# Performance work log

Measured on AMD Instinct MI355X. Metric: run time of the kernel, lower is better.

## Reference

```python
import jax, jax.numpy as jnp
import numpy as np

IN_F = 2048
OUT_F = 2048
BATCH = 16384
BASE_SPARSITY = 0.02
REVIVAL_DENSITY = 0.2   # rows for dead ('low') output neurons
RELIEF_DENSITY = 0.15   # cols for saturated ('high') input neurons
DEAD = np.arange(16)                      # 'low' extrema (row indices)
SATURATED = np.arange(100, 900, 100)      # 'high' extrema (col indices)


def _make_mask(key):
    k1, k2, k3 = jax.random.split(key, 3)
    base = (jax.random.uniform(k1, (OUT_F, IN_F)) < BASE_SPARSITY).astype(jnp.float32)
    patch = jnp.zeros((OUT_F, IN_F), jnp.float32)
    # dense-ish rows for dead output neurons
    row_patch = (jax.random.uniform(k2, (len(DEAD), IN_F)) < REVIVAL_DENSITY).astype(jnp.float32)
    patch = patch.at[jnp.asarray(DEAD), :].set(row_patch)
    # dense-ish cols for saturated input neurons (overwrite, matching torch order)
    col_patch = (jax.random.uniform(k3, (OUT_F, len(SATURATED))) < RELIEF_DENSITY).astype(jnp.float32)
    patch = patch.at[:, jnp.asarray(SATURATED)].set(col_patch)
    return jnp.maximum(base, patch)


def setup_inputs() -> dict:
    key = jax.random.key(0)
    kx, kw, km = jax.random.split(key, 3)
    x = jax.random.normal(kx, (BATCH, IN_F), dtype=jnp.float32)
    # kaiming_uniform_(a=sqrt(5)) -> U(-bound, bound), bound = sqrt(6/((1+a^2)*fan_in)) = 1/sqrt(fan_in)
    bound = 1.0 / np.sqrt(IN_F)
    weight = jax.random.uniform(kw, (OUT_F, IN_F), minval=-bound, maxval=bound, dtype=jnp.float32)
    bias = jnp.zeros((OUT_F,), jnp.float32)
    mask = _make_mask(km)
    return {"x": x, "weight": weight, "bias": bias, "mask": mask}


def reference(x, weight, bias, mask):
    # F.linear(x, weight * mask, bias): y = x @ (W*M)^T + b
    return jnp.einsum('bi,oi->bo', x, weight * mask) + bias
```

## Files before the change

kernel.cpp:

```cpp
#include <hip/hip_runtime.h>
#include <stdint.h>

#define BATCH 16384
#define IN_F 2048
#define OUT_F 2048

typedef unsigned short u16;
typedef __attribute__((ext_vector_type(8))) short bf16x8;
typedef __attribute__((ext_vector_type(4))) float f32x4;

__device__ __forceinline__ u16 f2bf(float f) {
  union { float f; uint32_t u; } v; v.f = f;
  uint32_t u = v.u;
  u += 0x7FFFu + ((u >> 16) & 1u);
  return (u16)(u >> 16);
}


__global__ void cvt_x_kernel(const float4* __restrict__ x, u16* __restrict__ out) {
  int i = blockIdx.x * 256 + threadIdx.x;
  float4 v = x[i];
  uint2 p;
  p.x = (uint32_t)f2bf(v.x) | ((uint32_t)f2bf(v.y) << 16);
  p.y = (uint32_t)f2bf(v.z) | ((uint32_t)f2bf(v.w) << 16);
  ((uint2*)out)[i] = p;
}

__global__ void cvt_w_kernel(const float4* __restrict__ w, const float4* __restrict__ m,
                             u16* __restrict__ out) {
  int i = blockIdx.x * 256 + threadIdx.x;
  float4 wv = w[i];
  float4 mv = m[i];
  uint2 p;
  p.x = (uint32_t)f2bf(wv.x * mv.x) | ((uint32_t)f2bf(wv.y * mv.y) << 16);
  p.y = (uint32_t)f2bf(wv.z * mv.z) | ((uint32_t)f2bf(wv.w * mv.w) << 16);
  ((uint2*)out)[i] = p;
}


__device__ __forceinline__ void async_cp16(const void* g, void* l) {
  __builtin_amdgcn_global_load_lds(
      (const __attribute__((address_space(1))) void*)g,
      (__attribute__((address_space(3))) void*)l,
      16, 0, 0);
}


__global__ __launch_bounds__(256) void gemm_bf16(const u16* __restrict__ A,
                                                 const u16* __restrict__ B,
                                                 const float* __restrict__ bias,
                                                 float* __restrict__ C) {
  __shared__ u16 lsA[128 * 32];
  __shared__ u16 lsB[128 * 32];
  const int K = IN_F, N = OUT_F;
  const int tid = threadIdx.x;
  const int lane = tid & 63, wave = tid >> 6;
  const int waveM = (wave & 1) * 64, waveN = (wave >> 1) * 64;
  const long bm = (long)blockIdx.x * 128;
  const long bn = (long)blockIdx.y * 128;

  const int o1 = tid * 16;
  const int o2 = o1 + 4096;
  const int r1 = tid >> 2, r2 = r1 + 64;
  const int c = tid & 3;
  const int cs1 = c ^ ((r1 >> 1) & 3);
  const int cs2 = c ^ ((r2 >> 1) & 3);
  const u16* gA1 = A + (bm + r1) * K + cs1 * 8;
  const u16* gA2 = A + (bm + r2) * K + cs2 * 8;
  const u16* gB1 = B + (bn + r1) * K + cs1 * 8;
  const u16* gB2 = B + (bn + r2) * K + cs2 * 8;
  char* lA1 = (char*)lsA + o1;
  char* lA2 = (char*)lsA + o2;
  char* lB1 = (char*)lsB + o1;
  char* lB2 = (char*)lsB + o2;

  f32x4 acc[4][4];
#pragma unroll
  for (int i = 0; i < 4; i++)
#pragma unroll
    for (int j = 0; j < 4; j++)
#pragma unroll
      for (int r = 0; r < 4; r++) acc[i][j][r] = 0.0f;

  const int mrow = lane & 15;
  const int q = lane >> 4;

  for (int k0 = 0; k0 < K; k0 += 32) {
    async_cp16(gA1 + k0, lA1);
    async_cp16(gA2 + k0, lA2);
    async_cp16(gB1 + k0, lB1);
    async_cp16(gB2 + k0, lB2);
    __syncthreads();

    bf16x8 af[4], bfr[4];
#pragma unroll
    for (int i = 0; i < 4; i++) {
      const int rr = waveM + i * 16 + mrow;
      af[i] = *(const bf16x8*)&lsA[rr * 32 + (q ^ ((rr >> 1) & 3)) * 8];
    }
#pragma unroll
    for (int j = 0; j < 4; j++) {
      const int rr = waveN + j * 16 + mrow;
      bfr[j] = *(const bf16x8*)&lsB[rr * 32 + (q ^ ((rr >> 1) & 3)) * 8];
    }

#pragma unroll
    for (int i = 0; i < 4; i++)
#pragma unroll
      for (int j = 0; j < 4; j++)
        acc[i][j] = __builtin_amdgcn_mfma_f32_16x16x32_bf16(af[i], bfr[j], acc[i][j], 0, 0, 0);

    __syncthreads();
  }

  const int cn = lane & 15;
  const int crow = (lane >> 4) * 4;
#pragma unroll
  for (int j = 0; j < 4; j++) {
    const long n = bn + waveN + j * 16 + cn;
    const float bv = bias[n];
#pragma unroll
    for (int i = 0; i < 4; i++) {
      const long m0 = bm + waveM + i * 16 + crow;
      float* cp = C + m0 * N + n;
#pragma unroll
      for (int r = 0; r < 4; r++)
        cp[(long)r * N] = acc[i][j][r] + bv;
    }
  }
}


__global__ void naive_kernel(const float* __restrict__ x, const float* __restrict__ w,
                             const float* __restrict__ bias, const float* __restrict__ m,
                             float* __restrict__ out) {
  size_t idx = (size_t)blockIdx.x * 256 + threadIdx.x;
  int o = (int)(idx % OUT_F);
  size_t b = idx / OUT_F;
  float s = bias[o];
  const float* xr = x + b * IN_F;
  const float* wr = w + (size_t)o * IN_F;
  const float* mr = m + (size_t)o * IN_F;
  for (int k = 0; k < IN_F; k++) s += xr[k] * wr[k] * mr[k];
  out[idx] = s;
}

extern "C" void kernel_launch(void* const* d_in, const int* in_sizes, int n_in,
                              void* d_out, int out_size, void* d_ws, size_t ws_size,
                              hipStream_t stream) {
  const float* x = (const float*)d_in[0];
  const float* w = (const float*)d_in[1];
  const float* bias = (const float*)d_in[2];
  const float* mask = (const float*)d_in[3];
  float* out = (float*)d_out;

  const size_t xb_elems = (size_t)BATCH * IN_F;
  const size_t wm_elems = (size_t)OUT_F * IN_F;
  const size_t need = (xb_elems + wm_elems) * sizeof(u16);

  if (ws_size >= need) {
    u16* xb = (u16*)d_ws;
    u16* wm = xb + xb_elems;
    cvt_x_kernel<<<(uint32_t)(xb_elems / 4 / 256), 256, 0, stream>>>((const float4*)x, xb);
    cvt_w_kernel<<<(uint32_t)(wm_elems / 4 / 256), 256, 0, stream>>>((const float4*)w,
                                                                     (const float4*)mask, wm);
    gemm_bf16<<<dim3(BATCH / 128, OUT_F / 128), 256, 0, stream>>>(xb, wm, bias, out);
  } else {
    naive_kernel<<<(uint32_t)(((size_t)BATCH * OUT_F) / 256), 256, 0, stream>>>(x, w, bias, mask, out);
  }
}
```

Before: 407.2 us.

## Fuse fp32-to-bf16 conversion of x into GEMM tile loading

Removes the separate pass that converted x to bf16 in workspace; the GEMM now async-copies fp32 x tiles into LDS and converts them to bf16 when building MFMA fragments. This avoids an extra full read and write of the large activation matrix, at the cost of doubled A-tile global/LDS traffic per block and extra pack instructions in the inner loop. Rounding changes from round-to-nearest-even to round-half-up.

```diff
diff --git a/kernel.cpp b/kernel.cpp
--- a/kernel.cpp
+++ b/kernel.cpp
@@ -16,15 +16,12 @@
   return (u16)(u >> 16);
 }
 
+__device__ __forceinline__ uint32_t pk_bf16(float a, float b) {
+  uint32_t ua = __float_as_uint(a) + 0x8000u;
+  uint32_t ub = __float_as_uint(b) + 0x8000u;
+  return __builtin_amdgcn_perm(ub, ua, 0x07060302u);
+}
 
-__global__ void cvt_x_kernel(const float4* __restrict__ x, u16* __restrict__ out) {
-  int i = blockIdx.x * 256 + threadIdx.x;
-  float4 v = x[i];
-  uint2 p;
-  p.x = (uint32_t)f2bf(v.x) | ((uint32_t)f2bf(v.y) << 16);
-  p.y = (uint32_t)f2bf(v.z) | ((uint32_t)f2bf(v.w) << 16);
-  ((uint2*)out)[i] = p;
-}
 
 __global__ void cvt_w_kernel(const float4* __restrict__ w, const float4* __restrict__ m,
                              u16* __restrict__ out) {
@@ -46,12 +43,12 @@
 }
 
 
-__global__ __launch_bounds__(256) void gemm_bf16(const u16* __restrict__ A,
+__global__ __launch_bounds__(256) void gemm_xf32(const float* __restrict__ A,
                                                  const u16* __restrict__ B,
                                                  const float* __restrict__ bias,
                                                  float* __restrict__ C) {
-  __shared__ u16 lsA[128 * 32];
-  __shared__ u16 lsB[128 * 32];
+  __shared__ float lsA[128 * 32];
+  __shared__ u16  lsB[128 * 32];
   const int K = IN_F, N = OUT_F;
   const int tid = threadIdx.x;
   const int lane = tid & 63, wave = tid >> 6;
@@ -59,20 +56,26 @@
   const long bm = (long)blockIdx.x * 128;
   const long bn = (long)blockIdx.y * 128;
 
-  const int o1 = tid * 16;
-  const int o2 = o1 + 4096;
-  const int r1 = tid >> 2, r2 = r1 + 64;
-  const int c = tid & 3;
-  const int cs1 = c ^ ((r1 >> 1) & 3);
-  const int cs2 = c ^ ((r2 >> 1) & 3);
-  const u16* gA1 = A + (bm + r1) * K + cs1 * 8;
-  const u16* gA2 = A + (bm + r2) * K + cs2 * 8;
-  const u16* gB1 = B + (bn + r1) * K + cs1 * 8;
-  const u16* gB2 = B + (bn + r2) * K + cs2 * 8;
-  char* lA1 = (char*)lsA + o1;
-  char* lA2 = (char*)lsA + o2;
-  char* lB1 = (char*)lsB + o1;
-  char* lB2 = (char*)lsB + o2;
+  const float* gA[4];
+  char* lA[4];
+#pragma unroll
+  for (int kk = 0; kk < 4; kk++) {
+    const int s = kk * 256 + tid;
+    const int r = s >> 3, c = s & 7;
+    const int cg = c ^ (r & 7);
+    gA[kk] = A + (bm + r) * K + cg * 4;
+    lA[kk] = (char*)lsA + s * 16;
+  }
+  const u16* gB[2];
+  char* lB[2];
+#pragma unroll
+  for (int kk = 0; kk < 2; kk++) {
+    const int s = kk * 256 + tid;
+    const int r = s >> 2, c = s & 3;
+    const int cg = c ^ ((r >> 1) & 3);
+    gB[kk] = B + (bn + r) * K + cg * 8;
+    lB[kk] = (char*)lsB + s * 16;
+  }
 
   f32x4 acc[4][4];
 #pragma unroll
@@ -84,19 +87,28 @@
 
   const int mrow = lane & 15;
   const int q = lane >> 4;
+  const int q2 = q * 2;
 
   for (int k0 = 0; k0 < K; k0 += 32) {
-    async_cp16(gA1 + k0, lA1);
-    async_cp16(gA2 + k0, lA2);
-    async_cp16(gB1 + k0, lB1);
-    async_cp16(gB2 + k0, lB2);
+#pragma unroll
+    for (int kk = 0; kk < 4; kk++) async_cp16(gA[kk] + k0, lA[kk]);
+#pragma unroll
+    for (int kk = 0; kk < 2; kk++) async_cp16(gB[kk] + k0, lB[kk]);
     __syncthreads();
 
     bf16x8 af[4], bfr[4];
 #pragma unroll
     for (int i = 0; i < 4; i++) {
       const int rr = waveM + i * 16 + mrow;
-      af[i] = *(const bf16x8*)&lsA[rr * 32 + (q ^ ((rr >> 1) & 3)) * 8];
+      const f32x4* rowp = (const f32x4*)lsA + rr * 8;
+      f32x4 f0 = rowp[q2 ^ (rr & 7)];
+      f32x4 f1 = rowp[(q2 + 1) ^ (rr & 7)];
+      union { uint32_t u[4]; bf16x8 v; } cv;
+      cv.u[0] = pk_bf16(f0[0], f0[1]);
+      cv.u[1] = pk_bf16(f0[2], f0[3]);
+      cv.u[2] = pk_bf16(f1[0], f1[1]);
+      cv.u[3] = pk_bf16(f1[2], f1[3]);
+      af[i] = cv.v;
     }
 #pragma unroll
     for (int j = 0; j < 4; j++) {
@@ -154,17 +166,14 @@
   const float* mask = (const float*)d_in[3];
   float* out = (float*)d_out;
 
-  const size_t xb_elems = (size_t)BATCH * IN_F;
   const size_t wm_elems = (size_t)OUT_F * IN_F;
-  const size_t need = (xb_elems + wm_elems) * sizeof(u16);
+  const size_t need = wm_elems * sizeof(u16);
 
   if (ws_size >= need) {
-    u16* xb = (u16*)d_ws;
-    u16* wm = xb + xb_elems;
-    cvt_x_kernel<<<(uint32_t)(xb_elems / 4 / 256), 256, 0, stream>>>((const float4*)x, xb);
+    u16* wm = (u16*)d_ws;
     cvt_w_kernel<<<(uint32_t)(wm_elems / 4 / 256), 256, 0, stream>>>((const float4*)w,
                                                                      (const float4*)mask, wm);
-    gemm_bf16<<<dim3(BATCH / 128, OUT_F / 128), 256, 0, stream>>>(xb, wm, bias, out);
+    gemm_xf32<<<dim3(BATCH / 128, OUT_F / 128), 256, 0, stream>>>(x, wm, bias, out);
   } else {
     naive_kernel<<<(uint32_t)(((size_t)BATCH * OUT_F) / 256), 256, 0, stream>>>(x, w, bias, mask, out);
   }
```

New measurement: 437.5 us. +7.4%, slower.
